# Kernel tuning notes

Measured on AMD Instinct MI355X. Metric: run time of the kernel, lower is better.

## Reference

```python
import jax, jax.numpy as jnp
import numpy as np

NUM_AXES = 72
NUM_PARAMS = 12
D_MODEL = 1024
SEQ_LEN = 4096
MAX_PROP = 600
LN_EPS = 1e-5


def setup_inputs() -> dict:
    key = jax.random.key(0)
    k1, k2, k3 = jax.random.split(key, 3)
    hidden_states = jax.random.normal(k1, (1, SEQ_LEN, D_MODEL), dtype=jnp.float32)
    ln_gamma = jnp.ones((D_MODEL,), dtype=jnp.float32)
    ln_beta = jnp.zeros((D_MODEL,), dtype=jnp.float32)
    W = jax.random.normal(k2, (NUM_AXES * NUM_PARAMS, D_MODEL), dtype=jnp.float32) * (1.0 / np.sqrt(D_MODEL))
    b = jax.random.normal(k3, (NUM_AXES * NUM_PARAMS,), dtype=jnp.float32) * 0.02
    return {"hidden_states": hidden_states, "ln_gamma": ln_gamma, "ln_beta": ln_beta, "W": W, "b": b}


def reference(hidden_states, ln_gamma, ln_beta, W, b):
    S = hidden_states.shape[1]
    T = min(MAX_PROP, S)
    x = hidden_states[0]  # (S, D)
    # LayerNorm
    mu = jnp.mean(x, axis=-1, keepdims=True)
    var = jnp.mean((x - mu) ** 2, axis=-1, keepdims=True)
    h = (x - mu) * jax.lax.rsqrt(var + LN_EPS) * ln_gamma + ln_beta
    # Linear -> (S, 12, 72)
    p = (h @ W.T + b).reshape(S, NUM_PARAMS, NUM_AXES)
    sp = jax.nn.softplus
    c = p[:, 4]; c_th = p[:, 5]; phi = p[:, 6]; phi_th = p[:, 7]  # (S, A)
    d = sp(p[:, 1]); k = d * d / 4.0 + sp(p[:, 0])
    d_th = sp(p[:, 3]); k_th = d_th * d_th / 4.0 + sp(p[:, 2])
    omega1 = jnp.sqrt(4.0 * k - d * d) / 2.0
    omega1_th = jnp.sqrt(4.0 * k_th - d_th * d_th) / 2.0
    t = jnp.arange(T, dtype=jnp.float32)[None, :, None]  # (1, T, 1)
    # damped sinusoids, (S, T, A)
    lin = c[:, None, :] * jnp.exp(-d[:, None, :] / 2.0 * t) * jnp.sin(omega1[:, None, :] * t + phi[:, None, :])
    ang = c_th[:, None, :] * jnp.exp(-d_th[:, None, :] / 2.0 * t) * jnp.sin(omega1_th[:, None, :] * t + phi_th[:, None, :])
    sig = lin + ang
    # overlap-add: out[pos] += sig[s, t] where pos = s + t, keep pos < S
    pos = (jnp.arange(S)[:, None] + jnp.arange(T)[None, :]).reshape(-1)  # (S*T,)
    vals = sig.reshape(-1, NUM_AXES)
    vals = jnp.where((pos < S)[:, None], vals, 0.0)
    pos_c = jnp.minimum(pos, S - 1)
    summed = jax.ops.segment_sum(vals, pos_c, num_segments=S).T  # (A, S)
    acc_base = p[:, 8].T
    acc_std = sp(p[:, 9]).T
    gyro_base = p[:, 10].T
    gyro_std = sp(p[:, 11]).T
    return (summed, acc_base, acc_std, gyro_base, gyro_std)
```

## Files before the change

kernel.cpp:

```cpp
#include <hip/hip_runtime.h>
#include <hip/hip_bf16.h>
#include <math.h>

#define S_LEN   4096
#define DMODEL  1024
#define NAX     72
#define NPAR    12
#define NCOL    864
#define NCOLP   896
#define TPROP   600
#define LN_EPS  1e-5f
#define EPS_CUT 5e-7f

typedef _Float16 half4 __attribute__((ext_vector_type(4)));
typedef _Float16 half8 __attribute__((ext_vector_type(8)));
typedef float    f32x4  __attribute__((ext_vector_type(4)));
typedef float    f32x2  __attribute__((ext_vector_type(2)));
typedef float    f32x16 __attribute__((ext_vector_type(16)));

#define GLOAD16(gp, lp)                                                        \
    __builtin_amdgcn_global_load_lds(                                          \
        (const __attribute__((address_space(1))) void*)(gp),                   \
        (__attribute__((address_space(3))) void*)(lp), 16, 0, 0)

__global__ __launch_bounds__(256) void k_lnw(
    const float* __restrict__ x, const float* __restrict__ gamma,
    const float* __restrict__ beta, const float* __restrict__ W,
    _Float16* __restrict__ h, _Float16* __restrict__ Wf)
{
    int tid = threadIdx.x;
    if (blockIdx.x >= S_LEN) {
        int t = (blockIdx.x - S_LEN) * 256 + tid;
        int row = t >> 7;
        int c0  = (t & 127) * 8;
        half8 o;
        if (row < NCOL) {
            const float4* p = (const float4*)(W + (size_t)row * DMODEL + c0);
            float4 a = p[0], b = p[1];
            o[0]=(_Float16)a.x; o[1]=(_Float16)a.y; o[2]=(_Float16)a.z; o[3]=(_Float16)a.w;
            o[4]=(_Float16)b.x; o[5]=(_Float16)b.y; o[6]=(_Float16)b.z; o[7]=(_Float16)b.w;
        } else {
            #pragma unroll
            for (int i = 0; i < 8; ++i) o[i] = (_Float16)0.f;
        }
        *(half8*)(Wf + (size_t)row * DMODEL + c0) = o;
        return;
    }
    int row = blockIdx.x;
    const float4* xr = (const float4*)(x + (size_t)row * DMODEL);
    float4 v = xr[tid];
    float s  = v.x + v.y + v.z + v.w;
    float sq = v.x*v.x + v.y*v.y + v.z*v.z + v.w*v.w;
    #pragma unroll
    for (int off = 1; off < 64; off <<= 1) {
        s  += __shfl_xor(s, off);
        sq += __shfl_xor(sq, off);
    }
    __shared__ float ls[4], lq[4];
    int wid = tid >> 6, lane = tid & 63;
    if (lane == 0) { ls[wid] = s; lq[wid] = sq; }
    __syncthreads();
    s  = ls[0] + ls[1] + ls[2] + ls[3];
    sq = lq[0] + lq[1] + lq[2] + lq[3];
    float mu  = s * (1.f / DMODEL);
    float var = sq * (1.f / DMODEL) - mu * mu;
    float rs  = rsqrtf(var + LN_EPS);
    float4 g = ((const float4*)gamma)[tid];
    float4 b = ((const float4*)beta)[tid];
    half4 o;
    o.x = (_Float16)((v.x - mu) * rs * g.x + b.x);
    o.y = (_Float16)((v.y - mu) * rs * g.y + b.y);
    o.z = (_Float16)((v.z - mu) * rs * g.z + b.z);
    o.w = (_Float16)((v.w - mu) * rs * g.w + b.w);
    ((half4*)(h + (size_t)row * DMODEL))[tid] = o;
}

__global__ __launch_bounds__(256) void k_gemm(
    const _Float16* __restrict__ A, const _Float16* __restrict__ B,
    const float* __restrict__ bias, float* __restrict__ P)
{
    __shared__ char smem[12288];
    char* smA = smem;
    char* smB = smem + 8192;

    int tid  = threadIdx.x;
    int lane = tid & 63;
    int wid  = tid >> 6;
    int wr   = wid >> 1, wc = wid & 1;
    int n0   = blockIdx.x * 64;
    int m0   = blockIdx.y * 128;

    int qa0 = tid, qa1 = tid + 256;
    int ar0 = qa0 >> 2, ac0 = (qa0 & 3) ^ ((ar0 >> 1) & 3);
    int ar1 = qa1 >> 2, ac1 = (qa1 & 3) ^ ((ar1 >> 1) & 3);
    int br  = tid >> 2, bc  = (tid & 3) ^ ((br >> 1) & 3);
    const _Float16* gA0 = A + (size_t)(m0 + ar0) * DMODEL + ac0 * 8;
    const _Float16* gA1 = A + (size_t)(m0 + ar1) * DMODEL + ac1 * 8;
    const _Float16* gB  = B + (size_t)(n0 + br)  * DMODEL + bc  * 8;

    int fr  = lane & 15;
    int chs = ((lane >> 4) ^ ((lane >> 1) & 3)) * 16;
    int aoff[4], boff[2];
    #pragma unroll
    for (int m = 0; m < 4; ++m) aoff[m] = (wr * 64 + m * 16 + fr) * 64 + chs;
    #pragma unroll
    for (int n = 0; n < 2; ++n) boff[n] = (wc * 32 + n * 16 + fr) * 64 + chs;

    f32x4 acc[4][2];
    #pragma unroll
    for (int m = 0; m < 4; ++m)
        #pragma unroll
        for (int n = 0; n < 2; ++n) acc[m][n] = (f32x4){0.f, 0.f, 0.f, 0.f};

    for (int k0 = 0; k0 < DMODEL; k0 += 32) {
        if (k0) __syncthreads();
        GLOAD16(gA0 + k0, smA + qa0 * 16);
        GLOAD16(gA1 + k0, smA + qa1 * 16);
        GLOAD16(gB  + k0, smB + tid * 16);
        __syncthreads();

        half8 af[4], bf[2];
        #pragma unroll
        for (int m = 0; m < 4; ++m) af[m] = *(const half8*)(smA + aoff[m]);
        #pragma unroll
        for (int n = 0; n < 2; ++n) bf[n] = *(const half8*)(smB + boff[n]);
        #pragma unroll
        for (int m = 0; m < 4; ++m)
            #pragma unroll
            for (int n = 0; n < 2; ++n)
                acc[m][n] = __builtin_amdgcn_mfma_f32_16x16x32_f16(
                                af[m], bf[n], acc[m][n], 0, 0, 0);
    }

    int rb = m0 + wr * 64 + (lane >> 4) * 4;
    #pragma unroll
    for (int n = 0; n < 2; ++n) {
        int col = n0 + wc * 32 + n * 16 + fr;
        float bv = (col < NCOL) ? bias[col] : 0.f;
        #pragma unroll
        for (int m = 0; m < 4; ++m) {
            int r0 = rb + m * 16;
            #pragma unroll
            for (int j = 0; j < 4; ++j)
                P[(size_t)(r0 + j) * NCOLP + col] = acc[m][n][j] + bv;
        }
    }
}

__device__ __forceinline__ float softplus_f(float x) {
    return fmaxf(x, 0.f) + log1pf(expf(-fabsf(x)));
}

__global__ __launch_bounds__(256) void k_params(
    const float* __restrict__ P, float* __restrict__ params,
    float* __restrict__ out)
{
    int g = blockIdx.x * 256 + threadIdx.x;
    if (g >= S_LEN * NAX) return;
    int s = g / NAX, a = g - s * NAX;
    const float* pr = P + (size_t)s * NCOLP + a;
    float p0  = pr[0*NAX], p1  = pr[1*NAX], p2  = pr[2*NAX], p3  = pr[3*NAX];
    float p4  = pr[4*NAX], p5  = pr[5*NAX], p6  = pr[6*NAX], p7  = pr[7*NAX];
    float p8  = pr[8*NAX], p9  = pr[9*NAX], p10 = pr[10*NAX], p11 = pr[11*NAX];

    float d  = softplus_f(p1), hd  = 0.5f * d;
    float w  = sqrtf(softplus_f(p0));
    float A  = 2.f * expf(-hd) * cosf(w);
    float B  = expf(-d);
    float d2 = softplus_f(p3), hd2 = 0.5f * d2;
    float w2 = sqrtf(softplus_f(p2));
    float A2 = 2.f * expf(-hd2) * cosf(w2);
    float B2 = expf(-d2);

    float4* pp = (float4*)(params + ((size_t)a * S_LEN + s) * 12);
    pp[0] = make_float4(A,   A2,  B,   B2);
    pp[1] = make_float4(p4,  p5,  hd,  hd2);
    pp[2] = make_float4(w,   w2,  p6,  p7);

    size_t o1 = (size_t)NAX * S_LEN;
    float* o = out + (size_t)a * S_LEN + s;
    o[1*o1] = p8;
    o[2*o1] = softplus_f(p9);
    o[3*o1] = p10;
    o[4*o1] = softplus_f(p11);
}

__device__ __forceinline__ f32x2 sin2(f32x2 v) {
    f32x2 r; r.x = __sinf(v.x); r.y = __sinf(v.y); return r;
}
__device__ __forceinline__ f32x2 exp2e(f32x2 v) {
    f32x2 r; r.x = __expf(v.x); r.y = __expf(v.y); return r;
}

#define PK_MUL_IP(d, s)                                                        \
    asm("v_pk_mul_f32 %0, %1, %0" : "+v"(d) : "v"(s))
#define PK_FMA_IP(d, a, b)                                                     \
    asm("v_pk_fma_f32 %0, %1, %2, %0" : "+v"(d) : "v"(a), "v"(b))

#define OSTEP2(V,K,KB) do {                                                    \
    PK_MUL_IP(xa, nB2v); PK_FMA_IP(xa, A2v, xb);  V[K]   += xa.x + xa.y;       \
    PK_MUL_IP(xb, nB2v); PK_FMA_IP(xb, A2v, xa);  V[K+1] += xb.x + xb.y; } while(0)

#define OSTEP2M(V,K,KB) do {                                                   \
    PK_MUL_IP(xa, nB2v); PK_FMA_IP(xa, A2v, xb);                               \
    V[K]   += (((KB)+(K))   <= iLim) ? (xa.x + xa.y) : 0.f;                    \
    PK_MUL_IP(xb, nB2v); PK_FMA_IP(xb, A2v, xa);                               \
    V[K+1] += (((KB)+(K)+1) <= iLim) ? (xb.x + xb.y) : 0.f; } while(0)

#define OSTEP2S(V,K,KB) do {                                                   \
    bool c0 = (((KB)+(K)) == lane);                                            \
    PK_MUL_IP(xa, nB2v); PK_FMA_IP(xa, A2v, xb);                               \
    xa.x = c0 ? x0.x : xa.x;   xa.y = c0 ? x0.y : xa.y;                        \
    xb.x = c0 ? xm1.x : xb.x;  xb.y = c0 ? xm1.y : xb.y;                       \
    V[K] += xa.x + xa.y;                                                       \
    bool c1 = (((KB)+(K)+1) == lane);                                          \
    PK_MUL_IP(xb, nB2v); PK_FMA_IP(xb, A2v, xa);                               \
    xb.x = c1 ? x0.x : xb.x;   xb.y = c1 ? x0.y : xb.y;                        \
    xa.x = c1 ? xm1.x : xa.x;  xa.y = c1 ? xm1.y : xa.y;                       \
    V[K+1] += xb.x + xb.y; } while(0)

#define RUN4P(OP)                                                              \
    { _Pragma("unroll") for (int k2=0;k2<8;++k2) OP(acc0,2*k2,0);              \
      _Pragma("unroll") for (int k2=0;k2<8;++k2) OP(acc1,2*k2,16);             \
      _Pragma("unroll") for (int k2=0;k2<8;++k2) OP(acc2,2*k2,32);             \
      _Pragma("unroll") for (int k2=0;k2<8;++k2) OP(acc3,2*k2,48); }

#define LOADP(J, Q0, Q1, Q2) do {                                              \
    int tb_ = ((J) - 1) * 64 + 1 + lane;                                       \
    int s_  = P0 - tb_;                                                        \
    int sc_ = (s_ >= 0 && tb_ <= 599) ? s_ : 0;                                \
    const float4* pp_ = (const float4*)(pbase + (size_t)sc_ * 12);             \
    Q0 = pp_[0]; Q1 = pp_[1]; Q2 = pp_[2]; } while(0)

__global__ __launch_bounds__(128, 3) void k_scan(
    const float* __restrict__ params, float* __restrict__ out)
{
    int tid  = threadIdx.x;
    int lane = tid & 63;
    int wid  = tid >> 6;
    int g    = (blockIdx.x & 7) * 288 + (blockIdx.x >> 3);
    int a    = g >> 5;
    int p    = g & 31;
    int tile = wid ? (63 - p) : p;
    int P0   = tile << 6;
    int nb   = tile < 10 ? tile : 10;

    f32x16 acc0 = {}, acc1 = {}, acc2 = {}, acc3 = {};

    const float* pbase = params + (size_t)a * S_LEN * 12;

    float4 n0, n1, n2;

    {
        int s = P0 + lane;
        const float4* pp = (const float4*)(pbase + (size_t)s * 12);
        float4 q0 = pp[0], q1 = pp[1], q2 = pp[2];
        if (nb >= 1) LOADP(1, n0, n1, n2);
        f32x2 A2v = {q0.x, q0.y};
        f32x2 nB2v = {-q0.z, -q0.w};
        f32x2 c2  = {q1.x, q1.y};
        f32x2 w2v = {q2.x, q2.y}, ph2 = {q2.z, q2.w};
        f32x2 ehd; ehd.x = rsqrtf(-nB2v.x); ehd.y = rsqrtf(-nB2v.y);
        f32x2 x0  = c2 * sin2(ph2);
        f32x2 xm1 = c2 * ehd * sin2(ph2 - w2v);
        f32x2 xa = {0.f, 0.f}, xb = {0.f, 0.f};
        RUN4P(OSTEP2S)
    }

    for (int j = 1; j <= nb; ++j) {
        float4 q0 = n0, q1 = n1, q2 = n2;
        if (j < nb) LOADP(j + 1, n0, n1, n2);

        int tb = (j - 1) * 64 + 1 + lane;
        bool ok = (tb <= 599);
        f32x2 A2v = {q0.x, q0.y};
        f32x2 nB2v = {-q0.z, -q0.w};
        f32x2 c2  = {q1.x, q1.y}, hd2 = {q1.z, q1.w};
        f32x2 w2v = {q2.x, q2.y}, ph2 = {q2.z, q2.w};
        if (!ok) { c2.x = 0.f; c2.y = 0.f; }
        f32x2 ehd; ehd.x = rsqrtf(-nB2v.x); ehd.y = rsqrtf(-nB2v.y);
        float fu = (float)(tb - 1);
        f32x2 e2 = c2 * exp2e(-hd2 * fu);

        bool alive = (fabsf(e2.x) > EPS_CUT) || (fabsf(e2.y) > EPS_CUT);
        if (__ballot(alive) == 0ULL) continue;

        f32x2 s1 = w2v * fu + ph2;
        f32x2 xb = e2 * sin2(s1);
        f32x2 xa = e2 * ehd * sin2(s1 - w2v);

        if (j <= 8) {
            RUN4P(OSTEP2)
        } else {
            int iLim = 599 - tb;
            RUN4P(OSTEP2M)
        }
    }

    bool s32 = (lane & 32) != 0;
    #pragma unroll
    for (int k = 0; k < 16; ++k) {
        float keep = s32 ? acc2[k] : acc0[k];
        float send = s32 ? acc0[k] : acc2[k];
        acc0[k] = keep + __shfl_xor(send, 32);
    }
    #pragma unroll
    for (int k = 0; k < 16; ++k) {
        float keep = s32 ? acc3[k] : acc1[k];
        float send = s32 ? acc1[k] : acc3[k];
        acc1[k] = keep + __shfl_xor(send, 32);
    }
    bool s16 = (lane & 16) != 0;
    #pragma unroll
    for (int k = 0; k < 16; ++k) {
        float keep = s16 ? acc1[k] : acc0[k];
        float send = s16 ? acc0[k] : acc1[k];
        acc0[k] = keep + __shfl_xor(send, 16);
    }
    bool s8 = (lane & 8) != 0;
    #pragma unroll
    for (int k = 0; k < 8; ++k) {
        float keep = s8 ? acc0[k + 8] : acc0[k];
        float send = s8 ? acc0[k]     : acc0[k + 8];
        acc0[k] = keep + __shfl_xor(send, 8);
    }
    bool s4 = (lane & 4) != 0;
    #pragma unroll
    for (int k = 0; k < 4; ++k) {
        float keep = s4 ? acc0[k + 4] : acc0[k];
        float send = s4 ? acc0[k]     : acc0[k + 4];
        acc0[k] = keep + __shfl_xor(send, 4);
    }
    bool s2 = (lane & 2) != 0;
    #pragma unroll
    for (int k = 0; k < 2; ++k) {
        float keep = s2 ? acc0[k + 2] : acc0[k];
        float send = s2 ? acc0[k]     : acc0[k + 2];
        acc0[k] = keep + __shfl_xor(send, 2);
    }
    bool s1 = (lane & 1) != 0;
    {
        float keep = s1 ? acc0[1] : acc0[0];
        float send = s1 ? acc0[0] : acc0[1];
        acc0[0] = keep + __shfl_xor(send, 1);
    }
    out[(size_t)a * S_LEN + P0 + lane] = acc0[0];
}

extern "C" void kernel_launch(void* const* d_in, const int* in_sizes, int n_in,
                              void* d_out, int out_size, void* d_ws, size_t ws_size,
                              hipStream_t stream)
{
    const float* x     = (const float*)d_in[0];
    const float* gamma = (const float*)d_in[1];
    const float* beta  = (const float*)d_in[2];
    const float* W     = (const float*)d_in[3];
    const float* bias  = (const float*)d_in[4];
    float* out = (float*)d_out;

    const size_t P_BYTES = (size_t)S_LEN * NCOLP * 4;
    char* ws = (char*)d_ws;
    float*    Pm     = (float*)ws;
    float*    params = (float*)(ws + P_BYTES);
    _Float16* hf     = (_Float16*)(ws + P_BYTES);
    _Float16* Wf     = (_Float16*)(ws + P_BYTES + (size_t)S_LEN * DMODEL * 2);

    k_lnw<<<dim3(S_LEN + NCOLP / 2), dim3(256), 0, stream>>>(x, gamma, beta, W, hf, Wf);
    k_gemm<<<dim3(NCOLP / 64, S_LEN / 128), dim3(256), 0, stream>>>(hf, Wf, bias, Pm);
    k_params<<<dim3((S_LEN * NAX + 255) / 256), dim3(256), 0, stream>>>(Pm, params, out);
    k_scan<<<dim3(2304), dim3(128), 0, stream>>>(params, out);
}
```

Baseline: 86.06 us.

## Compact surviving source rows into LDS list before overlap-add for far tiles

For source blocks beyond the second, each lane first tests whether its damped sinusoid is still above the cutoff and writes surviving lag indices into a per-wave LDS list using ballot and prefix rank. The accumulation loop then processes only the compacted live lanes, 64 at a time, instead of whole 64-lane blocks where most lanes are dead. This targets wasted divergent work from decayed sources, at the cost of an extra parameter-load pass and losing the software prefetch for those blocks. The first two blocks keep the dense path.

```diff
diff --git a/kernel.cpp b/kernel.cpp
--- a/kernel.cpp
+++ b/kernel.cpp
@@ -235,6 +235,7 @@
 __global__ __launch_bounds__(128, 3) void k_scan(
     const float* __restrict__ params, float* __restrict__ out)
 {
+    __shared__ unsigned short tbuf[2][512];
     int tid  = threadIdx.x;
     int lane = tid & 63;
     int wid  = tid >> 6;
@@ -267,17 +268,16 @@
         RUN4P(OSTEP2S)
     }
 
-    for (int j = 1; j <= nb; ++j) {
+    int jx = nb < 2 ? nb : 2;
+    for (int j = 1; j <= jx; ++j) {
         float4 q0 = n0, q1 = n1, q2 = n2;
-        if (j < nb) LOADP(j + 1, n0, n1, n2);
+        if (j < jx) LOADP(j + 1, n0, n1, n2);
 
         int tb = (j - 1) * 64 + 1 + lane;
-        bool ok = (tb <= 599);
         f32x2 A2v = {q0.x, q0.y};
         f32x2 nB2v = {-q0.z, -q0.w};
         f32x2 c2  = {q1.x, q1.y}, hd2 = {q1.z, q1.w};
         f32x2 w2v = {q2.x, q2.y}, ph2 = {q2.z, q2.w};
-        if (!ok) { c2.x = 0.f; c2.y = 0.f; }
         f32x2 ehd; ehd.x = rsqrtf(-nB2v.x); ehd.y = rsqrtf(-nB2v.y);
         float fu = (float)(tb - 1);
         f32x2 e2 = c2 * exp2e(-hd2 * fu);
@@ -288,10 +288,48 @@
         f32x2 s1 = w2v * fu + ph2;
         f32x2 xb = e2 * sin2(s1);
         f32x2 xa = e2 * ehd * sin2(s1 - w2v);
-
-        if (j <= 8) {
-            RUN4P(OSTEP2)
-        } else {
+        RUN4P(OSTEP2)
+    }
+
+    if (nb >= 3) {
+        int nA = 0;
+        for (int j = 3; j <= nb; ++j) {
+            int tb = (j - 1) * 64 + 1 + lane;
+            bool alive = false;
+            if (tb <= 599) {
+                const float4* pq = (const float4*)(pbase + (size_t)(P0 - tb) * 12);
+                float4 q1 = pq[1];
+                float fu = (float)(tb - 1);
+                float el = fabsf(q1.x) * __expf(-q1.z * fu);
+                float ea = fabsf(q1.y) * __expf(-q1.w * fu);
+                alive = (el > EPS_CUT) || (ea > EPS_CUT);
+            }
+            unsigned long long m = __ballot(alive);
+            if (alive) {
+                int rank = __popcll(m & ((1ULL << lane) - 1ULL));
+                tbuf[wid][nA + rank] = (unsigned short)tb;
+            }
+            nA += (int)__popcll(m);
+        }
+        __builtin_amdgcn_wave_barrier();
+
+        for (int base = 0; base < nA; base += 64) {
+            int idx = base + lane;
+            bool act = idx < nA;
+            int tb = act ? (int)tbuf[wid][idx] : 1;
+            const float4* pp = (const float4*)(pbase + (size_t)(P0 - tb) * 12);
+            float4 q0 = pp[0], q1 = pp[1], q2 = pp[2];
+            f32x2 A2v = {q0.x, q0.y};
+            f32x2 nB2v = {-q0.z, -q0.w};
+            f32x2 c2  = {q1.x, q1.y}, hd2 = {q1.z, q1.w};
+            f32x2 w2v = {q2.x, q2.y}, ph2 = {q2.z, q2.w};
+            if (!act) { c2.x = 0.f; c2.y = 0.f; }
+            f32x2 ehd; ehd.x = rsqrtf(-nB2v.x); ehd.y = rsqrtf(-nB2v.y);
+            float fu = (float)(tb - 1);
+            f32x2 e2 = c2 * exp2e(-hd2 * fu);
+            f32x2 s1 = w2v * fu + ph2;
+            f32x2 xb = e2 * sin2(s1);
+            f32x2 xa = e2 * ehd * sin2(s1 - w2v);
             int iLim = 599 - tb;
             RUN4P(OSTEP2M)
         }
```

After: 75.95 us. 11.7% less time.
